# Performance work log

Hardware: AMD Instinct MI355X
Metric: run time of the kernel (lower is better)

Reference implementation:

```python
import jax, jax.numpy as jnp
import numpy as np

TEMPERATURE = 0.07
EPS = 1e-12


def setup_inputs() -> dict:
    key = jax.random.key(0)
    k1, k2 = jax.random.split(key)
    B, D = 16384, 256
    return {
        "query_embeds": jax.random.normal(k1, (B, D), dtype=jnp.float32),
        "database_embeds": jax.random.normal(k2, (B, D), dtype=jnp.float32),
    }


def _l2_normalize(x, axis=1):
    # torch F.normalize: x / max(||x||, eps)
    norm = jnp.sqrt(jnp.sum(x * x, axis=axis, keepdims=True))
    return x / jnp.maximum(norm, EPS)


def reference(query_embeds, database_embeds):
    q = _l2_normalize(query_embeds, axis=1)   # [B, D]
    d = _l2_normalize(database_embeds, axis=1)  # [B, D]
    sim = jnp.einsum("bd,cd->bc", q, d) / TEMPERATURE  # [B, B]
    B = sim.shape[0]
    diag = jnp.diagonal(sim)  # logits at the correct (matching) label
    # CE over rows (q->d): -log_softmax(sim, axis=1)[i, i]
    lse_rows = jax.nn.logsumexp(sim, axis=1)
    loss_q2d = jnp.mean(lse_rows - diag)
    # CE over rows of sim.T == columns of sim (d->q)
    lse_cols = jax.nn.logsumexp(sim, axis=0)
    loss_d2q = jnp.mean(lse_cols - diag)
    return (loss_q2d + loss_d2q) / 2
```

## Files before the change

kernel.cpp:

```cpp
#include <hip/hip_runtime.h>
#include <hip/hip_bf16.h>
#include <cstdint>
#include <cstddef>

#define B_ROWS 16384
#define D_DIM  256
#define TEMP_INV 14.285714285714286f

#define NITER 16

using frag_cd = __attribute__((ext_vector_type(4))) float;
using i32x4   = __attribute__((ext_vector_type(4))) int;
using i32x8   = __attribute__((ext_vector_type(8))) int;

__device__ __forceinline__ void gld_lds16(const void* g, void* l) {
    __builtin_amdgcn_global_load_lds(
        (const __attribute__((address_space(1))) void*)g,
        (__attribute__((address_space(3))) void*)l,
        16, 0, 0);
}


__global__ __launch_bounds__(256) void norm_diag_kernel(
    const float* __restrict__ q, const float* __restrict__ d,
    unsigned int* __restrict__ qn, unsigned int* __restrict__ dn,
    float* __restrict__ diag,
    float* __restrict__ row_sums, float* __restrict__ col_sums,
    float* __restrict__ out) {
    const int b = blockIdx.x;
    if (b < 64)            row_sums[b * 256 + threadIdx.x] = 0.0f;
    else if (b < 128)      col_sums[(b - 64) * 256 + threadIdx.x] = 0.0f;
    else if (b == 128 && threadIdx.x == 0) out[0] = 0.0f;

    const int t    = threadIdx.x;
    const int lane = t & 63;
    const int w    = t >> 6;
    const int l15  = lane & 15;
    const int rw   = lane >> 4;
    const int r    = w * 4 + rw;
    const int row  = b * 16 + r;

    const float4* qr = (const float4*)(q + (size_t)row * D_DIM);
    const float4* dr = (const float4*)(d + (size_t)row * D_DIM);
    float4 qv[4], dv[4];
    float qss = 0.f, dss = 0.f, qd = 0.f;
#pragma unroll
    for (int p = 0; p < 4; ++p) {
        qv[p] = qr[l15 + 16 * p];
        dv[p] = dr[l15 + 16 * p];
        qss += qv[p].x*qv[p].x + qv[p].y*qv[p].y + qv[p].z*qv[p].z + qv[p].w*qv[p].w;
        dss += dv[p].x*dv[p].x + dv[p].y*dv[p].y + dv[p].z*dv[p].z + dv[p].w*dv[p].w;
        qd  += qv[p].x*dv[p].x + qv[p].y*dv[p].y + qv[p].z*dv[p].z + qv[p].w*dv[p].w;
    }
#pragma unroll
    for (int off = 1; off < 16; off <<= 1) {
        qss += __shfl_xor(qss, off);
        dss += __shfl_xor(dss, off);
        qd  += __shfl_xor(qd,  off);
    }
    const float qinv = 1.0f / fmaxf(sqrtf(qss), 1e-12f);
    const float dinv = 1.0f / fmaxf(sqrtf(dss), 1e-12f);

    __shared__ unsigned int qbuf[1024], dbuf[1024];
#pragma unroll
    for (int p = 0; p < 4; ++p) {
        const int jw = l15 + 16 * p;
        int qp = 0, dp = 0;
        qp = __builtin_amdgcn_cvt_pk_fp8_f32(qv[p].x * qinv, qv[p].y * qinv, qp, false);
        qp = __builtin_amdgcn_cvt_pk_fp8_f32(qv[p].z * qinv, qv[p].w * qinv, qp, true);
        dp = __builtin_amdgcn_cvt_pk_fp8_f32(dv[p].x * dinv, dv[p].y * dinv, dp, false);
        dp = __builtin_amdgcn_cvt_pk_fp8_f32(dv[p].z * dinv, dv[p].w * dinv, dp, true);
        const int c    = (jw & 31) >> 2;
        const int widx = ((jw >> 5) << 9) | ((c >> 2) << 8) | ((c & 3) << 6)
                       | (r << 2) | (jw & 3);
        qbuf[widx] = (unsigned int)qp;
        dbuf[widx] = (unsigned int)dp;
    }
    if (l15 == 0) diag[row] = qd * qinv * dinv * TEMP_INV;
    __syncthreads();
    ((uint4*)qn)[(size_t)b * 256 + t] = ((const uint4*)qbuf)[t];
    ((uint4*)dn)[(size_t)b * 256 + t] = ((const uint4*)dbuf)[t];
}

__global__ __launch_bounds__(256, 3) void gemm_lse_kernel(
    const unsigned char* __restrict__ qn, const unsigned char* __restrict__ dn,
    float* __restrict__ row_sums, float* __restrict__ col_sums) {
    __shared__ unsigned char ldsB[3][16384];

    const int t    = threadIdx.x;
    const int lane = t & 63;
    const int w    = t >> 6;
    const int l15  = lane & 15;
    const int quad = lane >> 4;

    const int id   = blockIdx.x;
    const int xcd  = id & 7;
    const int i    = id >> 3;
    const int chunk   = (xcd << 1) | (i & 1);
    const int rowg    = i >> 1;
    const int rowBase = rowg * 256;
    const int colChunkBase = chunk * 1024;

    union OpU { i32x8 v; i32x4 h[2]; };

    const unsigned char* aB = qn + ((size_t)((rowBase >> 4) + w * 4) << 12) + lane * 16;
    OpU a8[4][2];
#pragma unroll
    for (int mi = 0; mi < 4; ++mi)
#pragma unroll
        for (int kt = 0; kt < 2; ++kt) {
            a8[mi][kt].h[0] = *(const i32x4*)(aB + mi * 4096 + kt * 2048);
            a8[mi][kt].h[1] = *(const i32x4*)(aB + mi * 4096 + kt * 2048 + 1024);
        }

    const unsigned char* bG = dn + ((size_t)(colChunkBase >> 4) << 12);

#define STAGE(bufidx, j)                                                      \
    {                                                                          \
        const unsigned char* gsrc = bG + (size_t)(j) * 16384;                  \
        unsigned char* ldst = &ldsB[bufidx][0];                                \
        _Pragma("unroll")                                                      \
        for (int ii = 0; ii < 4; ++ii)                                         \
            gld_lds16(gsrc + ii * 4096 + t * 16, ldst + ii * 4096 + t * 16);   \
    }

    STAGE(0, 0)
    STAGE(1, 1)

    union RV { frag_cd v[4]; float f[16]; } rvu;
#pragma unroll
    for (int k = 0; k < 4; ++k) rvu.v[k] = (frag_cd){0.f, 0.f, 0.f, 0.f};

    const float C2 = TEMP_INV * 1.44269504088896f;
    const frag_cd zf = (frag_cd){0.f, 0.f, 0.f, 0.f};

    int cur = 0;
#pragma unroll 1
    for (int it = 0; it < NITER; ++it) {
        if (it == NITER - 1) asm volatile("s_waitcnt vmcnt(0)" ::: "memory");
        else                 asm volatile("s_waitcnt vmcnt(4)" ::: "memory");
        __builtin_amdgcn_s_barrier();
        asm volatile("" ::: "memory");

        const int nxt = (cur + 2 >= 3) ? cur - 1 : cur + 2;
        if (it + 2 < NITER) STAGE(nxt, it + 2)

        const unsigned char* bL = &ldsB[cur][0] + lane * 16;

        float cv[4] = {0.f, 0.f, 0.f, 0.f};

#pragma unroll
        for (int h = 0; h < 2; ++h) {
            const unsigned char* bH = bL + h * 2 * 4096;
            frag_cd acc[4][2];
            OpU b8[2];

#pragma unroll
            for (int ni = 0; ni < 2; ++ni) {
                b8[ni].h[0] = *(const i32x4*)(bH + ni * 4096);
                b8[ni].h[1] = *(const i32x4*)(bH + ni * 4096 + 1024);
            }
            __builtin_amdgcn_s_setprio(1);
#pragma unroll
            for (int mi = 0; mi < 4; ++mi)
#pragma unroll
                for (int ni = 0; ni < 2; ++ni)
                    acc[mi][ni] = __builtin_amdgcn_mfma_scale_f32_16x16x128_f8f6f4(
                        a8[mi][0].v, b8[ni].v, zf,
                        0, 0, 0, 0x7F7F7F7F, 0, 0x7F7F7F7F);
            __builtin_amdgcn_s_setprio(0);

#pragma unroll
            for (int ni = 0; ni < 2; ++ni) {
                b8[ni].h[0] = *(const i32x4*)(bH + ni * 4096 + 2048);
                b8[ni].h[1] = *(const i32x4*)(bH + ni * 4096 + 2048 + 1024);
            }
            __builtin_amdgcn_s_setprio(1);
#pragma unroll
            for (int mi = 0; mi < 4; ++mi)
#pragma unroll
                for (int ni = 0; ni < 2; ++ni)
                    acc[mi][ni] = __builtin_amdgcn_mfma_scale_f32_16x16x128_f8f6f4(
                        a8[mi][1].v, b8[ni].v, acc[mi][ni],
                        0, 0, 0, 0x7F7F7F7F, 0, 0x7F7F7F7F);
            __builtin_amdgcn_s_setprio(0);

#pragma unroll
            for (int mi = 0; mi < 4; ++mi)
#pragma unroll
                for (int ni = 0; ni < 2; ++ni) {
                    const frag_cd tt = acc[mi][ni] * C2 - C2;
                    frag_cd e;
#pragma unroll
                    for (int rr = 0; rr < 4; ++rr)
                        e[rr] = __builtin_amdgcn_exp2f(tt[rr]);
                    rvu.v[mi] += e;
                    cv[h * 2 + ni] += (e[0] + e[1]) + (e[2] + e[3]);
                }
        }

#pragma unroll
        for (int s = 0; s < 2; ++s) {
            const bool bb = (quad >> s) & 1;
#pragma unroll
            for (int k = 0; k < (2 >> s); ++k) {
                const float a0 = cv[2 * k], a1 = cv[2 * k + 1];
                const float keep = bb ? a1 : a0;
                const float send = bb ? a0 : a1;
                cv[k] = keep + __shfl_xor(send, 16 << s);
            }
        }
        atomicAdd(&col_sums[colChunkBase + it * 64 + quad * 16 + l15], cv[0]);

        cur = (cur + 1 >= 3) ? 0 : cur + 1;
    }
#undef STAGE

#pragma unroll
    for (int s = 0; s < 4; ++s) {
        const bool bb = (l15 >> s) & 1;
#pragma unroll
        for (int k = 0; k < (8 >> s); ++k) {
            const float a0 = rvu.f[2 * k], a1 = rvu.f[2 * k + 1];
            const float keep = bb ? a1 : a0;
            const float send = bb ? a0 : a1;
            rvu.f[k] = keep + __shfl_xor(send, 1 << s);
        }
    }
    atomicAdd(&row_sums[rowBase + w * 64 + (l15 >> 2) * 16 + quad * 4 + (l15 & 3)],
              rvu.f[0]);
}

__global__ __launch_bounds__(256) void finalize_kernel(
    const float* __restrict__ rs, const float* __restrict__ cs,
    const float* __restrict__ dg, float* __restrict__ out) {
    const int i = blockIdx.x * 256 + threadIdx.x;
    float s = logf(rs[i]) + logf(cs[i]) - 2.0f * dg[i];
#pragma unroll
    for (int off = 32; off; off >>= 1) s += __shfl_down(s, off);
    __shared__ float buf[4];
    if ((threadIdx.x & 63) == 0) buf[threadIdx.x >> 6] = s;
    __syncthreads();
    if (threadIdx.x == 0) {
        float tot = (buf[0] + buf[1] + buf[2] + buf[3]) / (2.0f * B_ROWS);
        if (blockIdx.x == 0) tot += TEMP_INV;
        atomicAdd(out, tot);
    }
}

extern "C" void kernel_launch(void* const* d_in, const int* in_sizes, int n_in,
                              void* d_out, int out_size, void* d_ws, size_t ws_size,
                              hipStream_t stream) {
    const float* q = (const float*)d_in[0];
    const float* d = (const float*)d_in[1];
    float* out = (float*)d_out;

    char* ws = (char*)d_ws;
    unsigned char* qn = (unsigned char*)ws;
    unsigned char* dn = qn + (size_t)B_ROWS * D_DIM;
    float* row_sums = (float*)(ws + 2 * (size_t)B_ROWS * D_DIM);
    float* col_sums = row_sums + B_ROWS;
    float* diag     = col_sums + B_ROWS;

    norm_diag_kernel<<<B_ROWS / 16, 256, 0, stream>>>(
        q, d, (unsigned int*)qn, (unsigned int*)dn, diag, row_sums, col_sums, out);
    gemm_lse_kernel<<<(B_ROWS / 256) * (B_ROWS / 1024), 256, 0, stream>>>(
        qn, dn, row_sums, col_sums);
    finalize_kernel<<<B_ROWS / 256, 256, 0, stream>>>(row_sums, col_sums, diag, out);
}
```

Baseline: 148.5 us.

## Software-pipeline exp epilogue of one half-tile behind MFMAs of the next

Splits each iteration's two column halves into separate accumulator sets (accA/accB) so the exp2/sum epilogue of the previous half runs while the next half's MFMAs issue, with the last epilogue drained after the loop. The aim is to overlap transcendental VALU work with matrix-core work. Column-sum reduction is also simplified to per-half butterfly shuffles with atomics from half the quads. Occupancy hint drops from 3 to 2 blocks per CU to make room for the doubled accumulator registers, which reduces latency hiding across waves.

```diff
diff --git a/kernel.cpp b/kernel.cpp
--- a/kernel.cpp
+++ b/kernel.cpp
@@ -82,7 +82,7 @@
     ((uint4*)dn)[(size_t)b * 256 + t] = ((const uint4*)dbuf)[t];
 }
 
-__global__ __launch_bounds__(256, 3) void gemm_lse_kernel(
+__global__ __launch_bounds__(256, 2) void gemm_lse_kernel(
     const unsigned char* __restrict__ qn, const unsigned char* __restrict__ dn,
     float* __restrict__ row_sums, float* __restrict__ col_sums) {
     __shared__ unsigned char ldsB[3][16384];
@@ -134,6 +134,67 @@
     const float C2 = TEMP_INV * 1.44269504088896f;
     const frag_cd zf = (frag_cd){0.f, 0.f, 0.f, 0.f};
 
+#define HALF(ACC, bH)                                                         \
+    {                                                                          \
+        OpU b8[2];                                                             \
+        _Pragma("unroll")                                                      \
+        for (int ni = 0; ni < 2; ++ni) {                                       \
+            b8[ni].h[0] = *(const i32x4*)((bH) + ni * 4096);                   \
+            b8[ni].h[1] = *(const i32x4*)((bH) + ni * 4096 + 1024);            \
+        }                                                                      \
+        __builtin_amdgcn_s_setprio(1);                                         \
+        _Pragma("unroll")                                                      \
+        for (int mi = 0; mi < 4; ++mi)                                         \
+            _Pragma("unroll")                                                  \
+            for (int ni = 0; ni < 2; ++ni)                                     \
+                ACC[mi][ni] = __builtin_amdgcn_mfma_scale_f32_16x16x128_f8f6f4(\
+                    a8[mi][0].v, b8[ni].v, zf,                                 \
+                    0, 0, 0, 0x7F7F7F7F, 0, 0x7F7F7F7F);                       \
+        __builtin_amdgcn_s_setprio(0);                                         \
+        _Pragma("unroll")                                                      \
+        for (int ni = 0; ni < 2; ++ni) {                                       \
+            b8[ni].h[0] = *(const i32x4*)((bH) + ni * 4096 + 2048);            \
+            b8[ni].h[1] = *(const i32x4*)((bH) + ni * 4096 + 3072);            \
+        }                                                                      \
+        __builtin_amdgcn_s_setprio(1);                                         \
+        _Pragma("unroll")                                                      \
+        for (int mi = 0; mi < 4; ++mi)                                         \
+            _Pragma("unroll")                                                  \
+            for (int ni = 0; ni < 2; ++ni)                                     \
+                ACC[mi][ni] = __builtin_amdgcn_mfma_scale_f32_16x16x128_f8f6f4(\
+                    a8[mi][1].v, b8[ni].v, ACC[mi][ni],                        \
+                    0, 0, 0, 0x7F7F7F7F, 0, 0x7F7F7F7F);                       \
+        __builtin_amdgcn_s_setprio(0);                                         \
+    }
+
+#define EPI(ACC, colbase)                                                     \
+    {                                                                          \
+        float cv0 = 0.f, cv1 = 0.f;                                            \
+        _Pragma("unroll")                                                      \
+        for (int mi = 0; mi < 4; ++mi) {                                       \
+            frag_cd tt = ACC[mi][0] * C2 - C2;                                 \
+            frag_cd e;                                                         \
+            _Pragma("unroll")                                                  \
+            for (int rr = 0; rr < 4; ++rr)                                     \
+                e[rr] = __builtin_amdgcn_exp2f(tt[rr]);                        \
+            rvu.v[mi] += e;                                                    \
+            cv0 += (e[0] + e[1]) + (e[2] + e[3]);                              \
+            tt = ACC[mi][1] * C2 - C2;                                         \
+            _Pragma("unroll")                                                  \
+            for (int rr = 0; rr < 4; ++rr)                                     \
+                e[rr] = __builtin_amdgcn_exp2f(tt[rr]);                        \
+            rvu.v[mi] += e;                                                    \
+            cv1 += (e[0] + e[1]) + (e[2] + e[3]);                              \
+        }                                                                      \
+        cv0 += __shfl_xor(cv0, 16); cv0 += __shfl_xor(cv0, 32);                \
+        cv1 += __shfl_xor(cv1, 16); cv1 += __shfl_xor(cv1, 32);                \
+        if (quad < 2)                                                          \
+            atomicAdd(&col_sums[(colbase) + quad * 16 + l15],                  \
+                      quad ? cv1 : cv0);                                       \
+    }
+
+    frag_cd accA[4][2], accB[4][2];
+
     int cur = 0;
 #pragma unroll 1
     for (int it = 0; it < NITER; ++it) {
@@ -147,74 +208,19 @@
 
         const unsigned char* bL = &ldsB[cur][0] + lane * 16;
 
-        float cv[4] = {0.f, 0.f, 0.f, 0.f};
-
-#pragma unroll
-        for (int h = 0; h < 2; ++h) {
-            const unsigned char* bH = bL + h * 2 * 4096;
-            frag_cd acc[4][2];
-            OpU b8[2];
-
-#pragma unroll
-            for (int ni = 0; ni < 2; ++ni) {
-                b8[ni].h[0] = *(const i32x4*)(bH + ni * 4096);
-                b8[ni].h[1] = *(const i32x4*)(bH + ni * 4096 + 1024);
-            }
-            __builtin_amdgcn_s_setprio(1);
-#pragma unroll
-            for (int mi = 0; mi < 4; ++mi)
-#pragma unroll
-                for (int ni = 0; ni < 2; ++ni)
-                    acc[mi][ni] = __builtin_amdgcn_mfma_scale_f32_16x16x128_f8f6f4(
-                        a8[mi][0].v, b8[ni].v, zf,
-                        0, 0, 0, 0x7F7F7F7F, 0, 0x7F7F7F7F);
-            __builtin_amdgcn_s_setprio(0);
-
-#pragma unroll
-            for (int ni = 0; ni < 2; ++ni) {
-                b8[ni].h[0] = *(const i32x4*)(bH + ni * 4096 + 2048);
-                b8[ni].h[1] = *(const i32x4*)(bH + ni * 4096 + 2048 + 1024);
-            }
-            __builtin_amdgcn_s_setprio(1);
-#pragma unroll
-            for (int mi = 0; mi < 4; ++mi)
-#pragma unroll
-                for (int ni = 0; ni < 2; ++ni)
-                    acc[mi][ni] = __builtin_amdgcn_mfma_scale_f32_16x16x128_f8f6f4(
-                        a8[mi][1].v, b8[ni].v, acc[mi][ni],
-                        0, 0, 0, 0x7F7F7F7F, 0, 0x7F7F7F7F);
-            __builtin_amdgcn_s_setprio(0);
-
-#pragma unroll
-            for (int mi = 0; mi < 4; ++mi)
-#pragma unroll
-                for (int ni = 0; ni < 2; ++ni) {
-                    const frag_cd tt = acc[mi][ni] * C2 - C2;
-                    frag_cd e;
-#pragma unroll
-                    for (int rr = 0; rr < 4; ++rr)
-                        e[rr] = __builtin_amdgcn_exp2f(tt[rr]);
-                    rvu.v[mi] += e;
-                    cv[h * 2 + ni] += (e[0] + e[1]) + (e[2] + e[3]);
-                }
-        }
-
-#pragma unroll
-        for (int s = 0; s < 2; ++s) {
-            const bool bb = (quad >> s) & 1;
-#pragma unroll
-            for (int k = 0; k < (2 >> s); ++k) {
-                const float a0 = cv[2 * k], a1 = cv[2 * k + 1];
-                const float keep = bb ? a1 : a0;
-                const float send = bb ? a0 : a1;
-                cv[k] = keep + __shfl_xor(send, 16 << s);
-            }
-        }
-        atomicAdd(&col_sums[colChunkBase + it * 64 + quad * 16 + l15], cv[0]);
+        HALF(accA, bL)
+        if (it) EPI(accB, colChunkBase + (it - 1) * 64 + 32)
+
+        HALF(accB, bL + 8192)
+        EPI(accA, colChunkBase + it * 64)
 
         cur = (cur + 1 >= 3) ? 0 : cur + 1;
     }
+    EPI(accB, colChunkBase + (NITER - 1) * 64 + 32)
+
 #undef STAGE
+#undef HALF
+#undef EPI
 
 #pragma unroll
     for (int s = 0; s < 4; ++s) {
```

Result: no change. 151.3 us (+1.9%).
